# Performance work log

Measured on AMD Instinct MI355X. Metric: run time of the kernel, lower is better.

The kernel has to match this reference:

```python
import jax, jax.numpy as jnp
import numpy as np

ALPHA, GAMMA = 0.25, 2.0
THR = 0.85            # soft_target_threshold
KL_EPS = 1e-6
FOCAL_EPS = 1e-8
VOC = 96              # len(vocab); index VOC is blank/pad


def setup_inputs() -> dict:
    key = jax.random.key(0)
    ks = jax.random.split(key, 6)
    bs, nq, n_pts, num_gt, L = 16, 200, 25, 32, 25
    return {
        "pred_logits": jax.random.normal(ks[0], (bs, nq, n_pts, 1), jnp.float32),
        "pred_ctrl_points": jax.random.uniform(ks[1], (bs, nq, n_pts, 2), jnp.float32),
        "pred_text_logits": jax.random.normal(ks[2], (bs, nq, n_pts, VOC + 1), jnp.float32),
        "tgt_ctrl_points": jax.random.uniform(ks[3], (bs, num_gt, n_pts, 2), jnp.float32),
        "tgt_texts": jax.random.randint(ks[4], (bs, num_gt, L), 0, VOC + 1),
        "centroids": jax.random.normal(ks[5], (VOC, 256), jnp.float32),
    }


def _cost_matrix(pred_logits, pred_ctrl_points, pred_text_logits,
                 tgt_ctrl_points, tgt_texts, centroids):
    bs, nq, n_pts, _ = pred_logits.shape
    num_gt = tgt_texts.shape[1]

    # ---- focal classification cost (mean over control points) ----
    out_prob = jax.nn.sigmoid(pred_logits.reshape(bs * nq, n_pts, -1))
    neg = (1.0 - ALPHA) * out_prob ** GAMMA * (-jnp.log1p(-(out_prob - FOCAL_EPS)))
    neg = (1.0 - ALPHA) * out_prob ** GAMMA * (-jnp.log(1.0 - out_prob + FOCAL_EPS))
    pos = ALPHA * (1.0 - out_prob) ** GAMMA * (-jnp.log(out_prob + FOCAL_EPS))
    cost_class = (pos[..., 0] - neg[..., 0]).mean(-1, keepdims=True)  # [bs*nq, 1]

    # ---- L1 cdist over flattened control points ----
    out_pts = pred_ctrl_points.reshape(bs * nq, n_pts * 2)
    tgt_pts = tgt_ctrl_points.reshape(bs * num_gt, n_pts * 2)
    cost_kpts = jnp.abs(out_pts[:, None, :] - tgt_pts[None, :, :]).sum(-1)  # [bs*nq, bs*num_gt]

    # ---- linguistic KL-div cost (per-batch block diagonal) ----
    probs = jax.nn.softmax(pred_text_logits, axis=-1)          # [bs,nq,n_pts,VOC+1]
    pred_avg = probs[..., :VOC].mean(axis=2)                   # [bs,nq,VOC]
    P = pred_avg + KL_EPS
    P = P / P.sum(-1, keepdims=True)
    logP = jnp.log(P)

    # soft target distribution per character (generate_soft_target_sequence)
    cn = centroids / jnp.linalg.norm(centroids, axis=-1, keepdims=True)
    soft_all = THR * jnp.eye(VOC, dtype=P.dtype) + (1.0 - THR) * jax.nn.softmax(cn @ cn.T, axis=-1)  # [VOC,VOC]

    mask = (tgt_texts != VOC)                                  # [bs,num_gt,L]
    lengths = mask.sum(-1)                                     # [bs,num_gt]
    per_char = soft_all[jnp.clip(tgt_texts, 0, VOC - 1)]       # [bs,num_gt,L,VOC]
    tgt_avg = (per_char * mask[..., None]).sum(2) / jnp.maximum(lengths, 1)[..., None].astype(P.dtype)
    T = tgt_avg + KL_EPS
    T = T / T.sum(-1, keepdims=True)                           # [bs,num_gt,VOC]

    # KL(T || P) = sum T*logT - sum T*logP, vectorized over (query, gt)
    kl = (T * jnp.log(T)).sum(-1)[:, None, :] - jnp.einsum('bqv,bgv->bqg', logP, T)  # [bs,nq,num_gt]
    kl = jnp.where(lengths[:, None, :] == 0, 100.0, kl)

    # place per-batch blocks on the diagonal of the global cost matrix
    eye = jnp.eye(bs, dtype=kl.dtype)
    cost_text = jnp.einsum('bqg,bc->bqcg', kl, eye).reshape(bs * nq, bs * num_gt)

    C = 1.0 * cost_class + 1.0 * cost_kpts + 1.0 * cost_text   # class/coord/text weights = 1
    return C.reshape(bs, nq, bs * num_gt)


def reference(pred_logits, pred_ctrl_points, pred_text_logits,
              tgt_ctrl_points, tgt_texts, centroids):
    return _cost_matrix(pred_logits, pred_ctrl_points, pred_text_logits,
                        tgt_ctrl_points, tgt_texts, centroids)
```

## Files before the change

### kernel.cpp

```cpp
#include <hip/hip_runtime.h>

#define BS 16
#define NQ 200
#define NPTS 25
#define VOC 96
#define VOCP1 97
#define NGT 32
#define LSEQ 25
#define NCOL (BS*NGT)
#define NBQ (BS*NQ)
#define KL_EPS 1e-6f
#define FOCAL_EPS 1e-8f

#define NB_CDIST 400
#define NB_SOFT VOC
#define NB_LOGP NBQ
#define NB_K1 (NB_CDIST + NB_SOFT + NB_LOGP)

__global__ __launch_bounds__(256) void K1(
        const float* __restrict__ pred_logits,
        const float* __restrict__ pred_ctrl,
        const float* __restrict__ pred_text_logits,
        const float* __restrict__ tgt_ctrl,
        const float* __restrict__ centroids,
        float* __restrict__ logP,
        float* __restrict__ soft,
        float* __restrict__ out)
{
    __shared__ __align__(16) float smem[64 * 52 * 2 + 64];
    const int tid = threadIdx.x;
    const int bid = blockIdx.x;

    if (bid < NB_CDIST) {
        const int cid = bid;
        const int r0  = (cid >> 3) * 64;
        const int c0  = (cid & 7) * 64;
        float (*s_p)[52] = (float (*)[52])smem;
        float (*s_t)[52] = (float (*)[52])(smem + 3328);
        float* s_cc = smem + 6656;

        const float* pg = pred_ctrl + (size_t)r0 * 50;
        const float* tg = tgt_ctrl + (size_t)c0 * 50;
        for (int i = tid; i < 64 * 50; i += 256) {
            int r = i / 50, d = i - r * 50;
            s_p[r][d] = pg[i];
            s_t[r][d] = tg[i];
        }
        {
            const int row4 = tid >> 2, q4 = tid & 3;
            float cc = 0.f;
            for (int p = q4; p < NPTS; p += 4) {
                float x  = pred_logits[(size_t)(r0 + row4) * NPTS + p];
                float pr = 1.f / (1.f + __expf(-x));
                float pos = 0.25f * (1.f - pr) * (1.f - pr) * (-__logf(pr + FOCAL_EPS));
                float neg = 0.75f * pr * pr * (-__logf(1.f - pr + FOCAL_EPS));
                cc += pos - neg;
            }
            cc += __shfl_xor(cc, 1, 4);
            cc += __shfl_xor(cc, 2, 4);
            if (q4 == 0) s_cc[row4] = cc * (1.0f / NPTS);
        }
        __syncthreads();

        const int tx = tid & 15;
        const int ty = tid >> 4;
        float acc[4][4];
        #pragma unroll
        for (int i = 0; i < 4; i++)
            #pragma unroll
            for (int j = 0; j < 4; j++) acc[i][j] = 0.f;

        #pragma unroll
        for (int k = 0; k < 48; k += 4) {
            float4 p[4], t[4];
            #pragma unroll
            for (int i = 0; i < 4; i++) p[i] = *(const float4*)&s_p[ty * 4 + i][k];
            #pragma unroll
            for (int j = 0; j < 4; j++) t[j] = *(const float4*)&s_t[tx + 16 * j][k];
            #pragma unroll
            for (int i = 0; i < 4; i++)
                #pragma unroll
                for (int j = 0; j < 4; j++)
                    acc[i][j] += fabsf(p[i].x - t[j].x) + fabsf(p[i].y - t[j].y)
                               + fabsf(p[i].z - t[j].z) + fabsf(p[i].w - t[j].w);
        }
        {
            float2 p[4], t[4];
            #pragma unroll
            for (int i = 0; i < 4; i++) p[i] = *(const float2*)&s_p[ty * 4 + i][48];
            #pragma unroll
            for (int j = 0; j < 4; j++) t[j] = *(const float2*)&s_t[tx + 16 * j][48];
            #pragma unroll
            for (int i = 0; i < 4; i++)
                #pragma unroll
                for (int j = 0; j < 4; j++)
                    acc[i][j] += fabsf(p[i].x - t[j].x) + fabsf(p[i].y - t[j].y);
        }

        #pragma unroll
        for (int i = 0; i < 4; i++) {
            const int row = ty * 4 + i;
            const float cc = s_cc[row];
            #pragma unroll
            for (int j = 0; j < 4; j++)
                out[(size_t)(r0 + row) * NCOL + c0 + tx + 16 * j] = acc[i][j] + cc;
        }

    } else if (bid < NB_CDIST + NB_SOFT) {
        const int i = bid - NB_CDIST;
        float4* s_c  = (float4*)smem;
        float* s_part = smem + 256;
        if (tid < 64)
            s_c[tid] = ((const float4*)(centroids + (size_t)i * 256))[tid];
        __syncthreads();

        float e = 0.f;
        if (tid < VOC) {
            float dij = 0.f, djj = 0.f, dii = 0.f;
            const float4* cj = (const float4*)(centroids + (size_t)tid * 256);
            #pragma unroll 4
            for (int k = 0; k < 64; k++) {
                float4 b = cj[k];
                float4 a = s_c[k];
                dij += a.x * b.x + a.y * b.y + a.z * b.z + a.w * b.w;
                djj += b.x * b.x + b.y * b.y + b.z * b.z + b.w * b.w;
                dii += a.x * a.x + a.y * a.y + a.z * a.z + a.w * a.w;
            }
            float sim = dij * rsqrtf(dii * djj);
            e = __expf(sim);
        }
        float s = e;
        #pragma unroll
        for (int off = 32; off; off >>= 1) s += __shfl_xor(s, off);
        const int wave = tid >> 6, lane = tid & 63;
        if (lane == 0) s_part[wave] = s;
        __syncthreads();
        float den = s_part[0] + s_part[1] + s_part[2] + s_part[3];
        if (tid < VOC) {
            float v = 0.15f * e / den;
            if (tid == i) v += 0.85f;
            soft[i * VOC + tid] = v;
        }

    } else {
        const int bq   = bid - (NB_CDIST + NB_SOFT);
        const int wave = tid >> 6, lane = tid & 63;
        float* s_acc = smem;
        float* s_p96 = smem + 388;

        const float* tl = pred_text_logits + (size_t)bq * NPTS * VOCP1;

        float e0[7], e1[7];
        #pragma unroll
        for (int k = 0; k < 6; k++) {
            const float* row = tl + (size_t)(wave + 4 * k) * VOCP1;
            e0[k] = row[lane];
            e1[k] = (lane < 33) ? row[64 + lane] : 0.f;
        }
        if (wave == 0) {
            const float* row = tl + (size_t)24 * VOCP1;
            e0[6] = row[lane];
            e1[6] = (lane < 33) ? row[64 + lane] : 0.f;
        }

        float acc0 = 0.f, acc1 = 0.f, acc96 = 0.f;
        #pragma unroll
        for (int k = 0; k < 6; k++) {
            float a = __expf(e0[k]);
            float b = (lane < 33) ? __expf(e1[k]) : 0.f;
            float s = a + b;
            #pragma unroll
            for (int off = 32; off; off >>= 1) s += __shfl_xor(s, off);
            float inv = __builtin_amdgcn_rcpf(s);
            acc0  += a * inv;
            acc1  += b * inv;
            acc96 += __shfl(b, 32) * inv;
        }
        if (wave == 0) {
            float a = __expf(e0[6]);
            float b = (lane < 33) ? __expf(e1[6]) : 0.f;
            float s = a + b;
            #pragma unroll
            for (int off = 32; off; off >>= 1) s += __shfl_xor(s, off);
            float inv = __builtin_amdgcn_rcpf(s);
            acc0  += a * inv;
            acc1  += b * inv;
            acc96 += __shfl(b, 32) * inv;
        }

        s_acc[wave * VOCP1 + lane] = acc0;
        if (lane < 33) s_acc[wave * VOCP1 + 64 + lane] = acc1;
        if (lane == 0) s_p96[wave] = acc96;
        __syncthreads();

        if (tid < VOC) {
            float a = (s_acc[tid] + s_acc[VOCP1 + tid]
                     + s_acc[2 * VOCP1 + tid] + s_acc[3 * VOCP1 + tid]) * (1.0f / NPTS);
            float S96 = s_p96[0] + s_p96[1] + s_p96[2] + s_p96[3];
            float denom = (25.0f - S96) * (1.0f / NPTS) + (float)VOC * KL_EPS;
            logP[(size_t)bq * VOC + tid] = __logf((a + KL_EPS) / denom);
        }
    }
}

__global__ __launch_bounds__(256) void K2(
        const int* __restrict__ tgt_texts,
        const float* __restrict__ soft,
        const float* __restrict__ logP,
        float* __restrict__ out)
{
    const int r0  = blockIdx.x * 8;
    const int b   = r0 / NQ;
    const int tid = threadIdx.x;
    __shared__ int   s_chars[NGT * LSEQ];
    __shared__ float s_lp[8][VOC];
    __shared__ float s_Tt[VOC][NGT + 1];
    __shared__ float s_tl[NGT];
    __shared__ int   s_len[NGT];

    for (int i = tid; i < NGT * LSEQ; i += 256)
        s_chars[i] = tgt_texts[b * NGT * LSEQ + i];
    for (int i = tid; i < 8 * VOC; i += 256)
        s_lp[i / VOC][i % VOC] = logP[(size_t)r0 * VOC + i];
    __syncthreads();

    const int grp = tid >> 5, sub = tid & 31;
    for (int g = grp; g < NGT; g += 8) {
        int len = 0;
        float a0 = 0.f, a1 = 0.f, a2 = 0.f;
        for (int l = 0; l < LSEQ; l++) {
            int t = s_chars[g * LSEQ + l];
            if (t != VOC) {
                len++;
                const float* sr = soft + t * VOC;
                a0 += sr[sub]; a1 += sr[sub + 32]; a2 += sr[sub + 64];
            }
        }
        float inv = 1.f / (float)(len > 0 ? len : 1);
        a0 *= inv; a1 *= inv; a2 *= inv;
        float s = a0 + a1 + a2;
        #pragma unroll
        for (int off = 16; off; off >>= 1) s += __shfl_xor(s, off, 32);
        float denom = s + (float)VOC * KL_EPS;
        float t0 = (a0 + KL_EPS) / denom;
        float t1 = (a1 + KL_EPS) / denom;
        float t2 = (a2 + KL_EPS) / denom;
        s_Tt[sub][g]      = t0;
        s_Tt[sub + 32][g] = t1;
        s_Tt[sub + 64][g] = t2;
        float tl = t0 * __logf(t0) + t1 * __logf(t1) + t2 * __logf(t2);
        #pragma unroll
        for (int off = 16; off; off >>= 1) tl += __shfl_xor(tl, off, 32);
        if (sub == 0) { s_tl[g] = tl; s_len[g] = len; }
    }
    __syncthreads();

    const int g = tid & 31, rs = tid >> 5;
    float d = 0.f;
    #pragma unroll 8
    for (int v = 0; v < VOC; v++) d += s_lp[rs][v] * s_Tt[v][g];
    float val = (s_len[g] == 0) ? 100.f : (s_tl[g] - d);
    size_t o = (size_t)(r0 + rs) * NCOL + b * NGT + g;
    out[o] += val;
}

extern "C" void kernel_launch(void* const* d_in, const int* in_sizes, int n_in,
                              void* d_out, int out_size, void* d_ws, size_t ws_size,
                              hipStream_t stream) {
    const float* pred_logits = (const float*)d_in[0];
    const float* pred_ctrl   = (const float*)d_in[1];
    const float* pred_text   = (const float*)d_in[2];
    const float* tgt_ctrl    = (const float*)d_in[3];
    const int*   tgt_texts   = (const int*)d_in[4];
    const float* centroids   = (const float*)d_in[5];
    float* out = (float*)d_out;

    float* ws   = (float*)d_ws;
    float* logP = ws;
    float* soft = logP + (size_t)NBQ * VOC;

    K1<<<NB_K1, 256, 0, stream>>>(pred_logits, pred_ctrl, pred_text,
                                  tgt_ctrl, centroids, logP, soft, out);
    K2<<<400, 256, 0, stream>>>(tgt_texts, soft, logP, out);
}
```

Baseline: 115.6 us.

## Map one query per wave for logP and read cdist preds from global

The text-softmax branch now gives each wavefront a whole query, four queries per block, instead of spreading one query's 25 points over four waves. This removes the LDS reduction and the __syncthreads, and cuts that branch's block count by four. The cdist branch no longer stages prediction rows in shared memory and loads them straight from global with float2 reads, so it uses less LDS. In exchange it makes repeated uncoalesced global loads that now rely on the cache.

Result: slower. 126.9 us (+9.7%).

```diff
diff --git a/kernel.cpp b/kernel.cpp
--- a/kernel.cpp
+++ b/kernel.cpp
@@ -14,7 +14,7 @@
 
 #define NB_CDIST 400
 #define NB_SOFT VOC
-#define NB_LOGP NBQ
+#define NB_LOGP (NBQ/4)
 #define NB_K1 (NB_CDIST + NB_SOFT + NB_LOGP)
 
 __global__ __launch_bounds__(256) void K1(
@@ -27,25 +27,19 @@
         float* __restrict__ soft,
         float* __restrict__ out)
 {
-    __shared__ __align__(16) float smem[64 * 52 * 2 + 64];
+    __shared__ __align__(16) float smem[64 * 50 + 64];
     const int tid = threadIdx.x;
     const int bid = blockIdx.x;
 
     if (bid < NB_CDIST) {
-        const int cid = bid;
-        const int r0  = (cid >> 3) * 64;
-        const int c0  = (cid & 7) * 64;
-        float (*s_p)[52] = (float (*)[52])smem;
-        float (*s_t)[52] = (float (*)[52])(smem + 3328);
-        float* s_cc = smem + 6656;
-
-        const float* pg = pred_ctrl + (size_t)r0 * 50;
+        const int r0  = (bid >> 3) * 64;
+        const int c0  = (bid & 7) * 64;
+        float (*s_t)[50] = (float (*)[50])smem;
+        float* s_cc = smem + 3200;
+
         const float* tg = tgt_ctrl + (size_t)c0 * 50;
-        for (int i = tid; i < 64 * 50; i += 256) {
-            int r = i / 50, d = i - r * 50;
-            s_p[r][d] = pg[i];
-            s_t[r][d] = tg[i];
-        }
+        for (int i = tid; i < 64 * 50; i += 256)
+            ((float*)s_t)[i] = tg[i];
         {
             const int row4 = tid >> 2, q4 = tid & 3;
             float cc = 0.f;
@@ -64,6 +58,11 @@
 
         const int tx = tid & 15;
         const int ty = tid >> 4;
+        const float* prow[4];
+        #pragma unroll
+        for (int i = 0; i < 4; i++)
+            prow[i] = pred_ctrl + (size_t)(r0 + ty * 4 + i) * 50;
+
         float acc[4][4];
         #pragma unroll
         for (int i = 0; i < 4; i++)
@@ -71,25 +70,12 @@
             for (int j = 0; j < 4; j++) acc[i][j] = 0.f;
 
         #pragma unroll
-        for (int k = 0; k < 48; k += 4) {
-            float4 p[4], t[4];
-            #pragma unroll
-            for (int i = 0; i < 4; i++) p[i] = *(const float4*)&s_p[ty * 4 + i][k];
-            #pragma unroll
-            for (int j = 0; j < 4; j++) t[j] = *(const float4*)&s_t[tx + 16 * j][k];
-            #pragma unroll
-            for (int i = 0; i < 4; i++)
-                #pragma unroll
-                for (int j = 0; j < 4; j++)
-                    acc[i][j] += fabsf(p[i].x - t[j].x) + fabsf(p[i].y - t[j].y)
-                               + fabsf(p[i].z - t[j].z) + fabsf(p[i].w - t[j].w);
-        }
-        {
+        for (int k = 0; k < 50; k += 2) {
             float2 p[4], t[4];
             #pragma unroll
-            for (int i = 0; i < 4; i++) p[i] = *(const float2*)&s_p[ty * 4 + i][48];
-            #pragma unroll
-            for (int j = 0; j < 4; j++) t[j] = *(const float2*)&s_t[tx + 16 * j][48];
+            for (int i = 0; i < 4; i++) p[i] = *(const float2*)(prow[i] + k);
+            #pragma unroll
+            for (int j = 0; j < 4; j++) t[j] = *(const float2*)&s_t[tx + 16 * j][k];
             #pragma unroll
             for (int i = 0; i < 4; i++)
                 #pragma unroll
@@ -143,62 +129,40 @@
         }
 
     } else {
-        const int bq   = bid - (NB_CDIST + NB_SOFT);
         const int wave = tid >> 6, lane = tid & 63;
-        float* s_acc = smem;
-        float* s_p96 = smem + 388;
-
+        const int bq   = (bid - (NB_CDIST + NB_SOFT)) * 4 + wave;
         const float* tl = pred_text_logits + (size_t)bq * NPTS * VOCP1;
 
-        float e0[7], e1[7];
-        #pragma unroll
-        for (int k = 0; k < 6; k++) {
-            const float* row = tl + (size_t)(wave + 4 * k) * VOCP1;
-            e0[k] = row[lane];
-            e1[k] = (lane < 33) ? row[64 + lane] : 0.f;
-        }
-        if (wave == 0) {
-            const float* row = tl + (size_t)24 * VOCP1;
-            e0[6] = row[lane];
-            e1[6] = (lane < 33) ? row[64 + lane] : 0.f;
-        }
-
         float acc0 = 0.f, acc1 = 0.f, acc96 = 0.f;
         #pragma unroll
-        for (int k = 0; k < 6; k++) {
-            float a = __expf(e0[k]);
-            float b = (lane < 33) ? __expf(e1[k]) : 0.f;
-            float s = a + b;
-            #pragma unroll
-            for (int off = 32; off; off >>= 1) s += __shfl_xor(s, off);
-            float inv = __builtin_amdgcn_rcpf(s);
-            acc0  += a * inv;
-            acc1  += b * inv;
-            acc96 += __shfl(b, 32) * inv;
-        }
-        if (wave == 0) {
-            float a = __expf(e0[6]);
-            float b = (lane < 33) ? __expf(e1[6]) : 0.f;
-            float s = a + b;
-            #pragma unroll
-            for (int off = 32; off; off >>= 1) s += __shfl_xor(s, off);
-            float inv = __builtin_amdgcn_rcpf(s);
-            acc0  += a * inv;
-            acc1  += b * inv;
-            acc96 += __shfl(b, 32) * inv;
-        }
-
-        s_acc[wave * VOCP1 + lane] = acc0;
-        if (lane < 33) s_acc[wave * VOCP1 + 64 + lane] = acc1;
-        if (lane == 0) s_p96[wave] = acc96;
-        __syncthreads();
-
-        if (tid < VOC) {
-            float a = (s_acc[tid] + s_acc[VOCP1 + tid]
-                     + s_acc[2 * VOCP1 + tid] + s_acc[3 * VOCP1 + tid]) * (1.0f / NPTS);
-            float S96 = s_p96[0] + s_p96[1] + s_p96[2] + s_p96[3];
-            float denom = (25.0f - S96) * (1.0f / NPTS) + (float)VOC * KL_EPS;
-            logP[(size_t)bq * VOC + tid] = __logf((a + KL_EPS) / denom);
+        for (int g0 = 0; g0 < NPTS; g0 += 5) {
+            float a[5], b[5];
+            #pragma unroll
+            for (int j = 0; j < 5; j++) {
+                const float* row = tl + (size_t)(g0 + j) * VOCP1;
+                a[j] = row[lane];
+                b[j] = (lane < 33) ? row[64 + lane] : 0.f;
+            }
+            #pragma unroll
+            for (int j = 0; j < 5; j++) {
+                float ea = __expf(a[j]);
+                float eb = (lane < 33) ? __expf(b[j]) : 0.f;
+                float s = ea + eb;
+                #pragma unroll
+                for (int off = 32; off; off >>= 1) s += __shfl_xor(s, off);
+                float inv = __builtin_amdgcn_rcpf(s);
+                acc0  += ea * inv;
+                acc1  += eb * inv;
+                acc96 += __shfl(eb, 32) * inv;
+            }
+        }
+
+        float denom = (25.0f - acc96) * (1.0f / NPTS) + (float)VOC * KL_EPS;
+        float a0 = acc0 * (1.0f / NPTS);
+        logP[(size_t)bq * VOC + lane] = __logf((a0 + KL_EPS) / denom);
+        if (lane < 32) {
+            float a1 = acc1 * (1.0f / NPTS);
+            logP[(size_t)bq * VOC + 64 + lane] = __logf((a1 + KL_EPS) / denom);
         }
     }
 }
```
